# Kernel tuning notes

Hardware: AMD Instinct MI355X
Metric: run time of the kernel (lower is better)

The kernel has to match this reference:

```python
import jax, jax.numpy as jnp
import numpy as np

H = 512      # hidden_size / feature_dim (hard-coded in Net)
H2 = 256     # hidden // 2 in encoder stem
V = 32000    # vocab_size = out_shape[0]
EPS = 1e-5   # BatchNorm eps (torch default)


def _conv(x, w, stride, pad, groups=1):
    return jax.lax.conv_general_dilated(
        x, w, (stride, stride), ((pad, pad), (pad, pad)),
        feature_group_count=groups,
        dimension_numbers=('NCHW', 'OIHW', 'NCHW'))


def _bn(x, g, b):
    # training-mode BatchNorm: biased batch statistics over (N,H,W)
    m = jnp.mean(x, axis=(0, 2, 3), keepdims=True)
    v = jnp.mean((x - m) ** 2, axis=(0, 2, 3), keepdims=True)
    return (x - m) * jax.lax.rsqrt(v + EPS) * g[None, :, None, None] + b[None, :, None, None]


def _encoder(images, conv1_w, bn1_g, bn1_b, dw_w, pw_w, bn2_g, bn2_b,
             se_fc1_w, se_fc2_w, enc_fc_w, enc_fc_b):
    x = jax.nn.relu(_bn(_conv(images, conv1_w, 2, 1), bn1_g, bn1_b))   # [B,256,112,112]
    x = _conv(x, dw_w, 1, 1, groups=H2)                                 # depthwise 3x3
    x = _conv(x, pw_w, 1, 0)                                            # pointwise -> [B,512,112,112]
    x = jax.nn.relu(_bn(x, bn2_g, bn2_b))
    y = jnp.mean(x, axis=(2, 3))                                        # SE squeeze [B,512]
    y = jax.nn.relu(y @ se_fc1_w.T) @ se_fc2_w.T
    x = x * jax.nn.sigmoid(y)[:, :, None, None]                         # SE excite
    f = jnp.mean(x, axis=(2, 3))                                        # AdaptiveAvgPool2d(1)
    return f @ enc_fc_w.T + enc_fc_b                                    # [B,512]


def _decode(feats, inputs, embed, q_w, k_w, v_w,
            gru_w_ih, gru_w_hh, gru_b_ih, gru_b_hh, fc_w, fc_b):
    B = feats.shape[0]
    # Attention over a single feature 'key' (r=1): softmax over one element
    # is exactly 1, so ctx = v(feats), independent of h and of t. q_w/k_w
    # therefore do not influence the output (their gradients are exactly 0).
    ctx = feats @ v_w.T                                                 # [B,512]
    embs = jnp.take(embed, inputs, axis=0)                              # [B,T,512]
    h0 = jnp.zeros((B, H), feats.dtype)

    def step(h, emb_t):
        x = jnp.concatenate([emb_t, ctx], axis=-1)                      # [B,1024]
        gi = x @ gru_w_ih.T + gru_b_ih                                  # [B,1536]
        gh = h @ gru_w_hh.T + gru_b_hh
        ir, iz, inn = jnp.split(gi, 3, axis=-1)
        hr, hz, hn = jnp.split(gh, 3, axis=-1)
        r = jax.nn.sigmoid(ir + hr)
        z = jax.nn.sigmoid(iz + hz)
        n = jnp.tanh(inn + r * hn)
        h_new = (1.0 - z) * n + z * h                                   # torch GRUCell update
        return h_new, h_new @ fc_w.T + fc_b                             # per-step logits [B,V]

    _, logits = jax.lax.scan(step, h0, jnp.swapaxes(embs, 0, 1))        # [T,B,V]
    return jnp.swapaxes(logits, 0, 1)                                   # [B,T,V]


def setup_inputs() -> dict:
    key = jax.random.key(0)
    ks = jax.random.split(key, 16)
    s = 0.02
    B, Tc = 16, 33
    return {
        'images': jax.random.normal(ks[0], (B, 3, 224, 224), jnp.float32),
        'captions': jax.random.randint(ks[1], (B, Tc), 0, V),
        'conv1_w': jax.random.normal(ks[2], (H2, 3, 3, 3), jnp.float32) * s,
        'bn1_g': jnp.ones((H2,), jnp.float32),
        'bn1_b': jnp.zeros((H2,), jnp.float32),
        'dw_w': jax.random.normal(ks[3], (H2, 1, 3, 3), jnp.float32) * s,
        'pw_w': jax.random.normal(ks[4], (H, H2, 1, 1), jnp.float32) * s,
        'bn2_g': jnp.ones((H,), jnp.float32),
        'bn2_b': jnp.zeros((H,), jnp.float32),
        'se_fc1_w': jax.random.normal(ks[5], (H // 4, H), jnp.float32) * s,
        'se_fc2_w': jax.random.normal(ks[6], (H, H // 4), jnp.float32) * s,
        'enc_fc_w': jax.random.normal(ks[7], (H, H), jnp.float32) * s,
        'enc_fc_b': jnp.zeros((H,), jnp.float32),
        'embed': jax.random.normal(ks[8], (V, H), jnp.float32) * s,
        'q_w': jax.random.normal(ks[9], (H, H), jnp.float32) * s,
        'k_w': jax.random.normal(ks[10], (H, H), jnp.float32) * s,
        'v_w': jax.random.normal(ks[11], (H, H), jnp.float32) * s,
        'gru_w_ih': jax.random.normal(ks[12], (3 * H, 2 * H), jnp.float32) * s,
        'gru_w_hh': jax.random.normal(ks[13], (3 * H, H), jnp.float32) * s,
        'gru_b_ih': jnp.zeros((3 * H,), jnp.float32),
        'gru_b_hh': jnp.zeros((3 * H,), jnp.float32),
        'fc_w': jax.random.normal(ks[14], (V, H), jnp.float32) * s,
        'fc_b': jnp.zeros((V,), jnp.float32),
    }


def reference(images, captions, conv1_w, bn1_g, bn1_b, dw_w, pw_w, bn2_g, bn2_b,
              se_fc1_w, se_fc2_w, enc_fc_w, enc_fc_b, embed, q_w, k_w, v_w,
              gru_w_ih, gru_w_hh, gru_b_ih, gru_b_hh, fc_w, fc_b):
    feats = _encoder(images, conv1_w, bn1_g, bn1_b, dw_w, pw_w, bn2_g, bn2_b,
                     se_fc1_w, se_fc2_w, enc_fc_w, enc_fc_b)
    inputs = captions[:, :-1]                                           # teacher forcing
    return _decode(feats, inputs, embed, q_w, k_w, v_w,
                   gru_w_ih, gru_w_hh, gru_b_ih, gru_b_hh, fc_w, fc_b)
```

## Files before the change

kernel.cpp:

```cpp
#include <hip/hip_runtime.h>

typedef unsigned int u32;
typedef unsigned short u16;
typedef unsigned long long u64;
typedef short bf16x8 __attribute__((ext_vector_type(8)));
typedef float f32x4 __attribute__((ext_vector_type(4)));

#define S1 12544
#define NSTAT 200704
#define EPS 1e-5f
#define AP 264

__device__ __forceinline__ u16 f2bf(float f) {
  union { float f; u32 u; } x; x.f = f;
  u32 r = x.u + 0x7fffu + ((x.u >> 16) & 1u);
  return (u16)(r >> 16);
}
__device__ __forceinline__ void bf2x2(u32 u, float& lo, float& hi) {
  union { u32 u; float f; } a, b;
  a.u = u << 16; b.u = u & 0xffff0000u;
  lo = a.f; hi = b.f;
}
__device__ __forceinline__ float sigm(float x) { return 1.f / (1.f + expf(-x)); }

#define CW 225
__global__ __launch_bounds__(256) void k_conv1(const float* __restrict__ img,
    const float* __restrict__ w, u16* __restrict__ out, float* __restrict__ stats) {
  int blk = blockIdx.x;
  int b = blk / 56, strip = blk - b * 56;
  int r0 = strip * 2;
  int c = threadIdx.x;
  __shared__ float simg[3 * 5 * CW];
  const float* ib = img + (size_t)b * 3 * 224 * 224;
  for (int i = c; i < 3 * 5 * CW; i += 256) {
    int ch = i / (5 * CW);
    int rem = i - ch * (5 * CW);
    int lr = rem / CW;
    int col = rem - lr * CW;
    int ih = 2 * r0 - 1 + lr;
    int iw = col - 1;
    float v = 0.f;
    if (ih >= 0 && ih < 224 && iw >= 0 && iw < 224) v = ib[((size_t)ch * 224 + ih) * 224 + iw];
    simg[i] = v;
  }
  float wr[27];
#pragma unroll
  for (int i = 0; i < 27; i++) wr[i] = w[c * 27 + i];
  __syncthreads();
  float s = 0.f, q = 0.f;
  for (int orow = 0; orow < 2; orow++) {
    int oh = r0 + orow;
    for (int ow = 0; ow < 112; ow++) {
      float acc = 0.f;
#pragma unroll
      for (int ch = 0; ch < 3; ch++)
#pragma unroll
        for (int dr = 0; dr < 3; dr++) {
          const float* rp = &simg[(ch * 5 + 2 * orow + dr) * CW + 2 * ow];
          acc = fmaf(wr[(ch * 3 + dr) * 3 + 0], rp[0], acc);
          acc = fmaf(wr[(ch * 3 + dr) * 3 + 1], rp[1], acc);
          acc = fmaf(wr[(ch * 3 + dr) * 3 + 2], rp[2], acc);
        }
      s += acc; q = fmaf(acc, acc, q);
      out[((size_t)(b * 112 + oh) * 112 + ow) * 256 + c] = f2bf(acc);
    }
  }
  atomicAdd(&stats[c], s);
  atomicAdd(&stats[256 + c], q);
}

__global__ void k_bnfin(const float* __restrict__ stats, const float* __restrict__ g,
                        const float* __restrict__ bb, float* __restrict__ par, int C, float invN) {
  int c = blockIdx.x * 256 + threadIdx.x;
  if (c < C) {
    float m = stats[c] * invN;
    float v = stats[C + c] * invN - m * m;
    float sc = g[c] * rsqrtf(v + EPS);
    par[c] = sc;
    par[C + c] = bb[c] - m * sc;
  }
}

__global__ void k_cvt4(const float* __restrict__ w, u16* __restrict__ o, int n4) {
  int i = blockIdx.x * 256 + threadIdx.x;
  if (i < n4) {
    float4 v = ((const float4*)w)[i];
    union { u16 h[4]; uint2 u; } pk;
    pk.h[0] = f2bf(v.x); pk.h[1] = f2bf(v.y); pk.h[2] = f2bf(v.z); pk.h[3] = f2bf(v.w);
    ((uint2*)o)[i] = pk.u;
  }
}

#define LD_COL(ohv, iwv, slot) do {                                          \
    int _oh = (ohv), _iw = (iwv);                                            \
  _Pragma("unroll")                                                          \
    for (int _dr = 0; _dr < 3; _dr++) {                                      \
      int _ih = _oh - 1 + _dr;                                               \
      float _x0 = 0.f, _x1 = 0.f, _x2 = 0.f, _x3 = 0.f;                      \
      if (_ih >= 0 && _ih < 112 && _iw >= 0 && _iw < 112) {                  \
        uint2 _v = *(const uint2*)(ib + ((size_t)(_ih * 112 + _iw)) * 256 + c4); \
        float _t0, _t1, _t2, _t3;                                            \
        bf2x2(_v.x, _t0, _t1); bf2x2(_v.y, _t2, _t3);                        \
        _x0 = fmaxf(fmaf(_t0, sc[0], sh[0]), 0.f);                           \
        _x1 = fmaxf(fmaf(_t1, sc[1], sh[1]), 0.f);                           \
        _x2 = fmaxf(fmaf(_t2, sc[2], sh[2]), 0.f);                           \
        _x3 = fmaxf(fmaf(_t3, sc[3], sh[3]), 0.f);                           \
      }                                                                      \
      act[_dr][slot][0] = _x0; act[_dr][slot][1] = _x1;                      \
      act[_dr][slot][2] = _x2; act[_dr][slot][3] = _x3;                      \
    }                                                                        \
  } while (0)

__global__ __launch_bounds__(256) void k_dws(const u16* __restrict__ cin,
    const float* __restrict__ bn1p, const float* __restrict__ dww, u16* __restrict__ out) {
  int tid = threadIdx.x;
  int wave = tid >> 6, lane = tid & 63;
  int c4 = lane * 4;
  int m0 = blockIdx.x * 64;
  int bimg = blockIdx.x / 196;
  float sc[4], sh[4], w9[4][9];
#pragma unroll
  for (int cc = 0; cc < 4; cc++) {
    sc[cc] = bn1p[c4 + cc];
    sh[cc] = bn1p[256 + c4 + cc];
#pragma unroll
    for (int i = 0; i < 9; i++) w9[cc][i] = dww[(c4 + cc) * 9 + i];
  }
  const u16* ib = cin + (size_t)bimg * S1 * 256;
  float act[3][3][4];
#pragma unroll
  for (int pp = 0; pp < 16; pp++) {
    int p = wave * 16 + pp;
    int s = m0 + p - bimg * S1;
    int oh = s / 112, ow = s - oh * 112;
    if (pp == 0 || ow == 0) {
      LD_COL(oh, ow - 1, (pp + 0) % 3);
      LD_COL(oh, ow,     (pp + 1) % 3);
      LD_COL(oh, ow + 1, (pp + 2) % 3);
    } else {
      LD_COL(oh, ow + 1, (pp + 2) % 3);
    }
    float a0 = 0.f, a1 = 0.f, a2 = 0.f, a3 = 0.f;
#pragma unroll
    for (int dr = 0; dr < 3; dr++)
#pragma unroll
      for (int dc = 0; dc < 3; dc++) {
        const int sl = (pp + dc) % 3;
        const int wi = dr * 3 + dc;
        a0 = fmaf(w9[0][wi], act[dr][sl][0], a0);
        a1 = fmaf(w9[1][wi], act[dr][sl][1], a1);
        a2 = fmaf(w9[2][wi], act[dr][sl][2], a2);
        a3 = fmaf(w9[3][wi], act[dr][sl][3], a3);
      }
    union { u16 h[4]; uint2 v; } pk;
    pk.h[0] = f2bf(a0); pk.h[1] = f2bf(a1);
    pk.h[2] = f2bf(a2); pk.h[3] = f2bf(a3);
    *(uint2*)(out + (size_t)(m0 + p) * 256 + c4) = pk.v;
  }
}

__global__ __launch_bounds__(256, 3) void k_pws(const u16* __restrict__ A,
    const u16* __restrict__ bwb, float* __restrict__ partials,
    const float* __restrict__ bn2p, int pass) {
  __shared__ u16 ash[64 * 256];
  int tid = threadIdx.x;
  int wave = tid >> 6, lane = tid & 63;
  int m0 = blockIdx.x * 64;
  {
    const char* gb = (const char*)(A + (size_t)m0 * 256);
    char* lb = (char*)ash;
#pragma unroll
    for (int i = 0; i < 8; i++) {
      int L = wave * 8192 + i * 1024 + lane * 16;
      int p = L >> 9;
      int gp = (L >> 4) & 31;
      int g = gp ^ (p & 7);
      uint4 v = *(const uint4*)(gb + (size_t)p * 512 + g * 16);
      *(uint4*)(lb + L) = v;
    }
  }
  __syncthreads();

  int quad = lane >> 4;
  int lr = lane & 15;
  int nbase = blockIdx.y * 256 + wave * 64;
  const char* ashb = (const char*)ash;
  f32x4 acc[4][4];
#pragma unroll
  for (int mt = 0; mt < 4; mt++)
#pragma unroll
    for (int nt = 0; nt < 4; nt++) acc[mt][nt] = (f32x4){0.f, 0.f, 0.f, 0.f};

#pragma unroll
  for (int ch = 0; ch < 8; ch++) {
    bf16x8 af[4];
#pragma unroll
    for (int mt = 0; mt < 4; mt++) {
      int row = mt * 16 + lr;
      int g = (ch * 4 + quad) ^ (row & 7);
      af[mt] = *(const bf16x8*)(ashb + row * 512 + g * 16);
    }
    bf16x8 bfr[4];
#pragma unroll
    for (int nt = 0; nt < 4; nt++)
      bfr[nt] = *(const bf16x8*)(bwb + (size_t)(nbase + nt * 16 + lr) * 256 + ch * 32 + quad * 8);
#pragma unroll
    for (int mt = 0; mt < 4; mt++)
#pragma unroll
      for (int nt = 0; nt < 4; nt++)
        acc[mt][nt] = __builtin_amdgcn_mfma_f32_16x16x32_bf16(af[mt], bfr[nt], acc[mt][nt], 0, 0, 0);
  }

  if (pass == 0) {
#pragma unroll
    for (int nt = 0; nt < 4; nt++) {
      float s = 0.f, q = 0.f;
#pragma unroll
      for (int mt = 0; mt < 4; mt++)
#pragma unroll
        for (int r = 0; r < 4; r++) {
          float v = acc[mt][nt][r];
          s += v; q = fmaf(v, v, q);
        }
      s += __shfl_xor(s, 16); s += __shfl_xor(s, 32);
      q += __shfl_xor(q, 16); q += __shfl_xor(q, 32);
      if (lane < 16) {
        int n = nbase + nt * 16 + lane;
        partials[(size_t)blockIdx.x * 1024 + n] = s;
        partials[(size_t)blockIdx.x * 1024 + 512 + n] = q;
      }
    }
  } else {
#pragma unroll
    for (int nt = 0; nt < 4; nt++) {
      int n = nbase + nt * 16 + lr;
      float scn = bn2p[n], shn = bn2p[512 + n];
      float s = 0.f;
#pragma unroll
      for (int mt = 0; mt < 4; mt++)
#pragma unroll
        for (int r = 0; r < 4; r++)
          s += fmaxf(fmaf(acc[mt][nt][r], scn, shn), 0.f);
      s += __shfl_xor(s, 16); s += __shfl_xor(s, 32);
      if (lane < 16)
        partials[(size_t)blockIdx.x * 512 + n] = s;
    }
  }
}

__global__ __launch_bounds__(256, 2) void k_pwpass(
    const u16* __restrict__ conv1out, const float* __restrict__ bn1p,
    const float* __restrict__ dww, const u16* __restrict__ bwb,
    float* __restrict__ partials, const float* __restrict__ bn2p, int pass) {
  __shared__ u16 ash[64 * AP];
  int tid = threadIdx.x;
  int wave = tid >> 6;
  int lane = tid & 63;
  int m0 = blockIdx.x * 64;
  int bimg = blockIdx.x / 196;
  {
    int c4 = lane * 4;
    float sc[4], sh[4], w9[4][9];
#pragma unroll
    for (int cc = 0; cc < 4; cc++) {
      sc[cc] = bn1p[c4 + cc];
      sh[cc] = bn1p[256 + c4 + cc];
#pragma unroll
      for (int i = 0; i < 9; i++) w9[cc][i] = dww[(c4 + cc) * 9 + i];
    }
    const u16* ib = conv1out + (size_t)bimg * S1 * 256;
    float act[3][3][4];
#pragma unroll
    for (int pp = 0; pp < 16; pp++) {
      int p = wave * 16 + pp;
      int s = m0 + p - bimg * S1;
      int oh = s / 112, ow = s - oh * 112;
      if (pp == 0 || ow == 0) {
        LD_COL(oh, ow - 1, (pp + 0) % 3);
        LD_COL(oh, ow,     (pp + 1) % 3);
        LD_COL(oh, ow + 1, (pp + 2) % 3);
      } else {
        LD_COL(oh, ow + 1, (pp + 2) % 3);
      }
      float a0 = 0.f, a1 = 0.f, a2 = 0.f, a3 = 0.f;
#pragma unroll
      for (int dr = 0; dr < 3; dr++)
#pragma unroll
        for (int dc = 0; dc < 3; dc++) {
          const int sl = (pp + dc) % 3;
          const int wi = dr * 3 + dc;
          a0 = fmaf(w9[0][wi], act[dr][sl][0], a0);
          a1 = fmaf(w9[1][wi], act[dr][sl][1], a1);
          a2 = fmaf(w9[2][wi], act[dr][sl][2], a2);
          a3 = fmaf(w9[3][wi], act[dr][sl][3], a3);
        }
      union { u16 h[4]; uint2 v; } pk;
      pk.h[0] = f2bf(a0); pk.h[1] = f2bf(a1);
      pk.h[2] = f2bf(a2); pk.h[3] = f2bf(a3);
      *(uint2*)(&ash[p * AP + c4]) = pk.v;
    }
  }
  __syncthreads();
  int quad = lane >> 4;
  int lr = lane & 15;
  int nbase = wave * 128;
  f32x4 acc[4][8];
#pragma unroll
  for (int mt = 0; mt < 4; mt++)
#pragma unroll
    for (int nt = 0; nt < 8; nt++) acc[mt][nt] = (f32x4){0.f, 0.f, 0.f, 0.f};
  for (int kk = 0; kk < 256; kk += 32) {
    bf16x8 af[4];
#pragma unroll
    for (int mt = 0; mt < 4; mt++)
      af[mt] = *(const bf16x8*)(&ash[(mt * 16 + lr) * AP + kk + quad * 8]);
    bf16x8 bfr[8];
#pragma unroll
    for (int nt = 0; nt < 8; nt++)
      bfr[nt] = *(const bf16x8*)(bwb + (size_t)(nbase + nt * 16 + lr) * 256 + kk + quad * 8);
#pragma unroll
    for (int mt = 0; mt < 4; mt++)
#pragma unroll
      for (int nt = 0; nt < 8; nt++)
        acc[mt][nt] = __builtin_amdgcn_mfma_f32_16x16x32_bf16(af[mt], bfr[nt], acc[mt][nt], 0, 0, 0);
  }
  if (pass == 0) {
#pragma unroll
    for (int nt = 0; nt < 8; nt++) {
      float s = 0.f, q = 0.f;
#pragma unroll
      for (int mt = 0; mt < 4; mt++)
#pragma unroll
        for (int r = 0; r < 4; r++) {
          float v = acc[mt][nt][r];
          s += v; q = fmaf(v, v, q);
        }
      s += __shfl_xor(s, 16); s += __shfl_xor(s, 32);
      q += __shfl_xor(q, 16); q += __shfl_xor(q, 32);
      if (lane < 16) {
        int n = nbase + nt * 16 + lane;
        partials[(size_t)blockIdx.x * 1024 + n] = s;
        partials[(size_t)blockIdx.x * 1024 + 512 + n] = q;
      }
    }
  } else {
#pragma unroll
    for (int nt = 0; nt < 8; nt++) {
      int n = nbase + nt * 16 + lr;
      float scn = bn2p[n], shn = bn2p[512 + n];
      float s = 0.f;
#pragma unroll
      for (int mt = 0; mt < 4; mt++)
#pragma unroll
        for (int r = 0; r < 4; r++)
          s += fmaxf(fmaf(acc[mt][nt][r], scn, shn), 0.f);
      s += __shfl_xor(s, 16); s += __shfl_xor(s, 32);
      if (lane < 16)
        partials[(size_t)blockIdx.x * 512 + n] = s;
    }
  }
}

__global__ __launch_bounds__(256) void k_red1(const float* __restrict__ P, float* __restrict__ P2) {
  int blk = blockIdx.x;
  int t = threadIdx.x;
  float4 s = {0.f, 0.f, 0.f, 0.f};
  for (int r = 0; r < 49; r++) {
    float4 v = *(const float4*)(P + ((size_t)(blk * 49 + r)) * 1024 + t * 4);
    s.x += v.x; s.y += v.y; s.z += v.z; s.w += v.w;
  }
  *(float4*)(P2 + (size_t)blk * 1024 + t * 4) = s;
}

__global__ void k_red_bn2(const float* __restrict__ P2, const float* __restrict__ g,
                          const float* __restrict__ bb, float* __restrict__ par) {
  int c = blockIdx.x * 256 + threadIdx.x;
  float s = 0.f, q = 0.f;
  for (int i = 0; i < 64; i++) {
    s += P2[(size_t)i * 1024 + c];
    q += P2[(size_t)i * 1024 + 512 + c];
  }
  float m = s * (1.f / (float)NSTAT);
  float v = q * (1.f / (float)NSTAT) - m * m;
  float sc = g[c] * rsqrtf(v + EPS);
  par[c] = sc;
  par[512 + c] = bb[c] - m * sc;
}

__global__ void k_red_y(const float* __restrict__ P, float* __restrict__ yb) {
  int idx = blockIdx.x * 256 + threadIdx.x;
  int b = idx >> 9, c = idx & 511;
  float s = 0.f;
  for (int i = 0; i < 196; i++) s += P[(size_t)(b * 196 + i) * 512 + c];
  yb[idx] = s;
}

__global__ __launch_bounds__(256) void k_se(const float* __restrict__ y,
    const float* __restrict__ se1, const float* __restrict__ se2,
    const float* __restrict__ encw, const float* __restrict__ encb,
    const float* __restrict__ vw, float* __restrict__ ctxb) {
  int b = blockIdx.x;
  int t = threadIdx.x;
  __shared__ __align__(16) float ybar[512];
  __shared__ __align__(16) float uu[128];
  __shared__ __align__(16) float ff[512];
  __shared__ __align__(16) float feats[512];
  for (int i = t; i < 512; i += 256) ybar[i] = y[b * 512 + i] * (1.f / 12544.f);
  __syncthreads();
  if (t < 128) {
    const float4* wr = (const float4*)(se1 + t * 512);
    const float4* xv = (const float4*)ybar;
    float a = 0.f;
    for (int k = 0; k < 128; k++) {
      float4 w4 = wr[k], x4 = xv[k];
      a = fmaf(w4.x, x4.x, a); a = fmaf(w4.y, x4.y, a);
      a = fmaf(w4.z, x4.z, a); a = fmaf(w4.w, x4.w, a);
    }
    uu[t] = fmaxf(a, 0.f);
  }
  __syncthreads();
  for (int c = t; c < 512; c += 256) {
    const float4* wr = (const float4*)(se2 + c * 128);
    const float4* xv = (const float4*)uu;
    float a = 0.f;
    for (int k = 0; k < 32; k++) {
      float4 w4 = wr[k], x4 = xv[k];
      a = fmaf(w4.x, x4.x, a); a = fmaf(w4.y, x4.y, a);
      a = fmaf(w4.z, x4.z, a); a = fmaf(w4.w, x4.w, a);
    }
    ff[c] = ybar[c] * sigm(a);
  }
  __syncthreads();
  for (int c = t; c < 512; c += 256) {
    const float4* wr = (const float4*)(encw + (size_t)c * 512);
    const float4* xv = (const float4*)ff;
    float a = encb[c];
    for (int k = 0; k < 128; k++) {
      float4 w4 = wr[k], x4 = xv[k];
      a = fmaf(w4.x, x4.x, a); a = fmaf(w4.y, x4.y, a);
      a = fmaf(w4.z, x4.z, a); a = fmaf(w4.w, x4.w, a);
    }
    feats[c] = a;
  }
  __syncthreads();
  for (int c = t; c < 512; c += 256) {
    const float4* wr = (const float4*)(vw + (size_t)c * 512);
    const float4* xv = (const float4*)feats;
    float a = 0.f;
    for (int k = 0; k < 128; k++) {
      float4 w4 = wr[k], x4 = xv[k];
      a = fmaf(w4.x, x4.x, a); a = fmaf(w4.y, x4.y, a);
      a = fmaf(w4.z, x4.z, a); a = fmaf(w4.w, x4.w, a);
    }
    ctxb[b * 512 + c] = a;
  }
}

__global__ __launch_bounds__(256) void k_gctx(const float* __restrict__ ctxb,
    const float* __restrict__ wih, const float* __restrict__ bih, float* __restrict__ gictx) {
  int lb = threadIdx.x >> 4;
  int lj = threadIdx.x & 15;
  int j = blockIdx.x * 16 + lj;
  const float4* wr = (const float4*)(wih + (size_t)j * 1024 + 512);
  const float4* xv = (const float4*)(ctxb + lb * 512);
  float a = bih[j];
#pragma unroll 4
  for (int k = 0; k < 128; k++) {
    float4 w4 = wr[k], x4 = xv[k];
    a = fmaf(w4.x, x4.x, a); a = fmaf(w4.y, x4.y, a);
    a = fmaf(w4.z, x4.z, a); a = fmaf(w4.w, x4.w, a);
  }
  gictx[lb * 1536 + j] = a;
}

__global__ __launch_bounds__(256) void k_gi3(const int* __restrict__ caps,
    const float* __restrict__ embed, const float* __restrict__ wih,
    const float* __restrict__ gictx, float* __restrict__ gi) {
  int wave = threadIdx.x >> 6, lane = threadIdx.x & 63;
  int j = blockIdx.x * 4 + wave;
  int t0 = blockIdx.y * 8;
  const float4* wr = (const float4*)(wih + (size_t)j * 1024 + lane * 8);
  float4 w0 = wr[0], w1 = wr[1];
  for (int tt = t0; tt < t0 + 8; tt++) {
#pragma unroll
    for (int bb = 0; bb < 16; bb += 8) {
      float4 x0[8], x1[8];
#pragma unroll
      for (int u = 0; u < 8; u++) {
        int tok = caps[(bb + u) * 33 + tt];
        const float4* xv = (const float4*)(embed + (size_t)tok * 512 + lane * 8);
        x0[u] = xv[0]; x1[u] = xv[1];
      }
#pragma unroll
      for (int u = 0; u < 8; u++) {
        float a = w0.x * x0[u].x;
        a = fmaf(w0.y, x0[u].y, a); a = fmaf(w0.z, x0[u].z, a); a = fmaf(w0.w, x0[u].w, a);
        a = fmaf(w1.x, x1[u].x, a); a = fmaf(w1.y, x1[u].y, a);
        a = fmaf(w1.z, x1[u].z, a); a = fmaf(w1.w, x1[u].w, a);
#pragma unroll
        for (int m = 1; m < 64; m <<= 1) a += __shfl_xor(a, m);
        if (lane == 0)
          gi[((size_t)tt * 16 + bb + u) * 1536 + j] = a + gictx[(bb + u) * 1536 + j];
      }
    }
  }
}

__global__ __launch_bounds__(192) void k_gru_step(const float* __restrict__ whh,
    const float* __restrict__ bhh, const float* __restrict__ gi_t,
    const float* __restrict__ h_in, float* __restrict__ h_out) {
  int g = blockIdx.x;
  int tid = threadIdx.x;
  int s = tid / 24;
  int r = tid - s * 24;
  int gate = r >> 3, lj = r & 7;
  int jj = g * 8 + lj;
  int R = gate * 512 + jj;
  float4 w[16];
  {
    const float4* wp = (const float4*)(whh + (size_t)R * 512 + s * 64);
#pragma unroll
    for (int i = 0; i < 16; i++) w[i] = wp[i];
  }
  __shared__ __align__(16) float hs[16][512];
  __shared__ float pr[8][24][16];

  {
    const float4* hp = (const float4*)h_in;
    float4* hd = (float4*)&hs[0][0];
    for (int i = tid; i < 2048; i += 192) hd[i] = hp[i];
  }
  __syncthreads();
#pragma unroll
  for (int b = 0; b < 16; b++) {
    const float4* hv = (const float4*)&hs[b][s * 64];
    float a = 0.f;
#pragma unroll
    for (int k = 0; k < 16; k++) {
      float4 w4 = w[k], h4 = hv[k];
      a = fmaf(w4.x, h4.x, a); a = fmaf(w4.y, h4.y, a);
      a = fmaf(w4.z, h4.z, a); a = fmaf(w4.w, h4.w, a);
    }
    pr[s][r][b] = a;
  }
  __syncthreads();
  if (tid < 128) {
    int b = tid >> 3, jl = tid & 7;
    int j = g * 8 + jl;
    float gh[3];
#pragma unroll
    for (int gg = 0; gg < 3; gg++) {
      int rr = gg * 8 + jl;
      float sum = bhh[gg * 512 + j];
#pragma unroll
      for (int ss = 0; ss < 8; ss++) sum += pr[ss][rr][b];
      gh[gg] = sum;
    }
    const float* gib = gi_t + (size_t)b * 1536;
    float rg = sigm(gib[j] + gh[0]);
    float z  = sigm(gib[j + 512] + gh[1]);
    float n  = tanhf(gib[j + 1024] + rg * gh[2]);
    float hp = hs[b][j];
    h_out[b * 512 + j] = (1.f - z) * n + z * hp;
  }
}

__global__ __launch_bounds__(256) void k_fc(const float* __restrict__ A,
    const u16* __restrict__ Bwb, const float* __restrict__ bias, float* __restrict__ out) {
  __shared__ u16 ash[128 * 136];
  int tid = threadIdx.x;
  int wave = tid >> 6;
  int lane = tid & 63;
  int quad = lane >> 4;
  int lr = lane & 15;
  int N0 = blockIdx.x * 256;
  int M0 = blockIdx.y * 128;
  f32x4 acc[8][4];
#pragma unroll
  for (int mf = 0; mf < 8; mf++)
#pragma unroll
    for (int nf = 0; nf < 4; nf++) acc[mf][nf] = (f32x4){0.f, 0.f, 0.f, 0.f};
  int arow = tid >> 1;
  int acol = (tid & 1) * 64;
  for (int kc = 0; kc < 512; kc += 128) {
#pragma unroll
    for (int j = 0; j < 16; j++) {
      float4 v = *(const float4*)(A + (size_t)(M0 + arow) * 512 + kc + acol + j * 4);
      union { u16 h[4]; uint2 u; } pk;
      pk.h[0] = f2bf(v.x); pk.h[1] = f2bf(v.y); pk.h[2] = f2bf(v.z); pk.h[3] = f2bf(v.w);
      *(uint2*)(&ash[arow * 136 + acol + j * 4]) = pk.u;
    }
    __syncthreads();
#pragma unroll
    for (int ks = 0; ks < 128; ks += 32) {
      bf16x8 af[8];
#pragma unroll
      for (int mf = 0; mf < 8; mf++)
        af[mf] = *(const bf16x8*)(&ash[(mf * 16 + lr) * 136 + ks + quad * 8]);
      bf16x8 bf[4];
#pragma unroll
      for (int nf = 0; nf < 4; nf++) {
        int n = N0 + wave * 64 + nf * 16 + lr;
        bf[nf] = *(const bf16x8*)(Bwb + (size_t)n * 512 + kc + ks + quad * 8);
      }
#pragma unroll
      for (int mf = 0; mf < 8; mf++)
#pragma unroll
        for (int nf = 0; nf < 4; nf++)
          acc[mf][nf] = __builtin_amdgcn_mfma_f32_16x16x32_bf16(af[mf], bf[nf], acc[mf][nf], 0, 0, 0);
    }
    __syncthreads();
  }
#pragma unroll
  for (int nf = 0; nf < 4; nf++) {
    int j = N0 + wave * 64 + nf * 16 + lr;
    float bv = bias[j];
#pragma unroll
    for (int mf = 0; mf < 8; mf++)
#pragma unroll
      for (int r = 0; r < 4; r++) {
        int m = M0 + mf * 16 + quad * 4 + r;
        int orow = (m & 15) * 32 + (m >> 4);
        out[(size_t)orow * 32000 + j] = acc[mf][nf][r] + bv;
      }
  }
}

extern "C" void kernel_launch(void* const* d_in, const int* in_sizes, int n_in,
                              void* d_out, int out_size, void* d_ws, size_t ws_size,
                              hipStream_t stream) {
  const float* images  = (const float*)d_in[0];
  const int*   caps    = (const int*)d_in[1];
  const float* conv1_w = (const float*)d_in[2];
  const float* bn1_g   = (const float*)d_in[3];
  const float* bn1_b   = (const float*)d_in[4];
  const float* dw_w    = (const float*)d_in[5];
  const float* pw_w    = (const float*)d_in[6];
  const float* bn2_g   = (const float*)d_in[7];
  const float* bn2_b   = (const float*)d_in[8];
  const float* se1     = (const float*)d_in[9];
  const float* se2     = (const float*)d_in[10];
  const float* encw    = (const float*)d_in[11];
  const float* encb    = (const float*)d_in[12];
  const float* embed   = (const float*)d_in[13];
  const float* vw      = (const float*)d_in[16];
  const float* wih     = (const float*)d_in[17];
  const float* whh     = (const float*)d_in[18];
  const float* bih     = (const float*)d_in[19];
  const float* bhh     = (const float*)d_in[20];
  const float* fcw     = (const float*)d_in[21];
  const float* fcb     = (const float*)d_in[22];
  float* out = (float*)d_out;

  const bool big = ws_size >= (size_t)230 * 1000 * 1000;

  char* ws = (char*)d_ws;
  size_t off = 0;
  auto alloc = [&](size_t bytes) {
    void* p = ws + off;
    off = (off + bytes + 255) & ~(size_t)255;
    return p;
  };
  u16* conv1out = (u16*)alloc((size_t)51380224 * 2);
  u16* fcwb     = (u16*)conv1out;
  u16* dwout    = big ? (u16*)alloc((size_t)51380224 * 2) : (u16*)nullptr;
  u16* bwb      = (u16*)alloc((size_t)131072 * 2);
  float* partials = (float*)alloc((size_t)3136 * 1024 * 4);
  float* p2     = (float*)alloc((size_t)64 * 1024 * 4);
  float* stats1 = (float*)alloc(512 * 4);
  float* h_all  = (float*)alloc((size_t)33 * 8192 * 4);
  float* bn1p   = (float*)alloc(512 * 4);
  float* bn2p   = (float*)alloc(1024 * 4);
  float* yb     = (float*)alloc(8192 * 4);
  float* ctxb   = (float*)alloc(8192 * 4);
  float* gictx  = (float*)alloc((size_t)16 * 1536 * 4);
  float* gi     = (float*)alloc((size_t)32 * 16 * 1536 * 4);
  (void)in_sizes; (void)n_in; (void)out_size;

  hipMemsetAsync(stats1, 0, 512 * 4, stream);
  hipMemsetAsync(h_all, 0, 8192 * 4, stream);

  k_conv1<<<896, 256, 0, stream>>>(images, conv1_w, conv1out, stats1);
  k_bnfin<<<1, 256, 0, stream>>>(stats1, bn1_g, bn1_b, bn1p, 256, 1.f / (float)NSTAT);
  k_cvt4<<<128, 256, 0, stream>>>(pw_w, bwb, 32768);

  if (big) {
    k_dws<<<3136, 256, 0, stream>>>(conv1out, bn1p, dw_w, dwout);
    k_cvt4<<<16000, 256, 0, stream>>>(fcw, fcwb, 4096000);
    dim3 gpw(3136, 2);
    k_pws<<<gpw, 256, 0, stream>>>(dwout, bwb, partials, bn2p, 0);
    k_red1<<<64, 256, 0, stream>>>(partials, p2);
    k_red_bn2<<<2, 256, 0, stream>>>(p2, bn2_g, bn2_b, bn2p);
    k_pws<<<gpw, 256, 0, stream>>>(dwout, bwb, partials, bn2p, 1);
  } else {
    k_pwpass<<<3136, 256, 0, stream>>>(conv1out, bn1p, dw_w, bwb, partials, bn2p, 0);
    k_red1<<<64, 256, 0, stream>>>(partials, p2);
    k_red_bn2<<<2, 256, 0, stream>>>(p2, bn2_g, bn2_b, bn2p);
    k_pwpass<<<3136, 256, 0, stream>>>(conv1out, bn1p, dw_w, bwb, partials, bn2p, 1);
    k_cvt4<<<16000, 256, 0, stream>>>(fcw, fcwb, 4096000);
  }
  k_red_y<<<32, 256, 0, stream>>>(partials, yb);
  k_se<<<16, 256, 0, stream>>>(yb, se1, se2, encw, encb, vw, ctxb);
  k_gctx<<<96, 256, 0, stream>>>(ctxb, wih, bih, gictx);
  dim3 ggi3(384, 4);
  k_gi3<<<ggi3, 256, 0, stream>>>(caps, embed, wih, gictx, gi);
  for (int t = 0; t < 32; t++)
    k_gru_step<<<64, 192, 0, stream>>>(whh, bhh, gi + (size_t)t * 16 * 1536,
                                       h_all + (size_t)t * 8192, h_all + (size_t)(t + 1) * 8192);
  dim3 gfc(125, 4);
  k_fc<<<gfc, 256, 0, stream>>>(h_all + 8192, fcwb, fcb, out);
}
```

Measured before the change: 1.273 ms.

## Transpose GRU input weights and rewrite embedding projection as LDS-staged GEMM

Adds a transpose kernel that lays out the embedding half of W_ih as [k][j]. The embedding projection is rewritten so each thread owns one output column and accumulates all 16 batch rows. The gathered embeddings are staged in shared memory, and weight reads are coalesced across lanes. This removes the per-output 64-lane shuffle reductions of the old kernel. The cost is an extra transpose pass, a 3MB buffer, and a grid of only 192 blocks, each running a 512-step serial loop.

```diff
diff --git a/kernel.cpp b/kernel.cpp
--- a/kernel.cpp
+++ b/kernel.cpp
@@ -108,7 +108,7 @@
       }                                                                      \
       act[_dr][slot][0] = _x0; act[_dr][slot][1] = _x1;                      \
       act[_dr][slot][2] = _x2; act[_dr][slot][3] = _x3;                      \
-    }                                                                        \
+    }                                                                      \
   } while (0)
 
 __global__ __launch_bounds__(256) void k_dws(const u16* __restrict__ cin,
@@ -473,37 +473,58 @@
   gictx[lb * 1536 + j] = a;
 }
 
-__global__ __launch_bounds__(256) void k_gi3(const int* __restrict__ caps,
-    const float* __restrict__ embed, const float* __restrict__ wih,
+__global__ __launch_bounds__(256) void k_trans(const float* __restrict__ wih,
+    float* __restrict__ wihT) {
+  __shared__ float tile[32][33];
+  int tx = threadIdx.x & 31, ty = threadIdx.x >> 5;
+  int j0 = blockIdx.x * 32, k0 = blockIdx.y * 32;
+#pragma unroll
+  for (int i = 0; i < 4; i++)
+    tile[ty + i * 8][tx] = wih[(size_t)(j0 + ty + i * 8) * 1024 + k0 + tx];
+  __syncthreads();
+#pragma unroll
+  for (int i = 0; i < 4; i++)
+    wihT[(size_t)(k0 + ty + i * 8) * 1536 + j0 + tx] = tile[tx][ty + i * 8];
+}
+
+__global__ __launch_bounds__(256) void k_gi4(const int* __restrict__ caps,
+    const float* __restrict__ embed, const float* __restrict__ wihT,
     const float* __restrict__ gictx, float* __restrict__ gi) {
-  int wave = threadIdx.x >> 6, lane = threadIdx.x & 63;
-  int j = blockIdx.x * 4 + wave;
-  int t0 = blockIdx.y * 8;
-  const float4* wr = (const float4*)(wih + (size_t)j * 1024 + lane * 8);
-  float4 w0 = wr[0], w1 = wr[1];
-  for (int tt = t0; tt < t0 + 8; tt++) {
-#pragma unroll
-    for (int bb = 0; bb < 16; bb += 8) {
-      float4 x0[8], x1[8];
-#pragma unroll
-      for (int u = 0; u < 8; u++) {
-        int tok = caps[(bb + u) * 33 + tt];
-        const float4* xv = (const float4*)(embed + (size_t)tok * 512 + lane * 8);
-        x0[u] = xv[0]; x1[u] = xv[1];
-      }
-#pragma unroll
-      for (int u = 0; u < 8; u++) {
-        float a = w0.x * x0[u].x;
-        a = fmaf(w0.y, x0[u].y, a); a = fmaf(w0.z, x0[u].z, a); a = fmaf(w0.w, x0[u].w, a);
-        a = fmaf(w1.x, x1[u].x, a); a = fmaf(w1.y, x1[u].y, a);
-        a = fmaf(w1.z, x1[u].z, a); a = fmaf(w1.w, x1[u].w, a);
-#pragma unroll
-        for (int m = 1; m < 64; m <<= 1) a += __shfl_xor(a, m);
-        if (lane == 0)
-          gi[((size_t)tt * 16 + bb + u) * 1536 + j] = a + gictx[(bb + u) * 1536 + j];
-      }
-    }
-  }
+  __shared__ __align__(16) float semb[512][16];
+  int tid = threadIdx.x;
+  int t = blockIdx.y;
+  for (int i = tid; i < 8192; i += 256) {
+    int k = i >> 4, b = i & 15;
+    int tok = caps[b * 33 + t];
+    semb[k][b] = embed[(size_t)tok * 512 + k];
+  }
+  __syncthreads();
+  int wave = tid >> 6, lane = tid & 63;
+  int j = (blockIdx.x * 4 + wave) * 64 + lane;
+  float acc[16];
+#pragma unroll
+  for (int b = 0; b < 16; b++) acc[b] = 0.f;
+  for (int k = 0; k < 512; k += 2) {
+    float wv0 = wihT[(size_t)k * 1536 + j];
+    float wv1 = wihT[(size_t)(k + 1) * 1536 + j];
+    const f32x4* e0 = (const f32x4*)&semb[k][0];
+    const f32x4* e1 = (const f32x4*)&semb[k + 1][0];
+#pragma unroll
+    for (int q = 0; q < 4; q++) {
+      f32x4 a0 = e0[q], a1 = e1[q];
+      acc[q * 4 + 0] = fmaf(wv0, a0[0], acc[q * 4 + 0]);
+      acc[q * 4 + 1] = fmaf(wv0, a0[1], acc[q * 4 + 1]);
+      acc[q * 4 + 2] = fmaf(wv0, a0[2], acc[q * 4 + 2]);
+      acc[q * 4 + 3] = fmaf(wv0, a0[3], acc[q * 4 + 3]);
+      acc[q * 4 + 0] = fmaf(wv1, a1[0], acc[q * 4 + 0]);
+      acc[q * 4 + 1] = fmaf(wv1, a1[1], acc[q * 4 + 1]);
+      acc[q * 4 + 2] = fmaf(wv1, a1[2], acc[q * 4 + 2]);
+      acc[q * 4 + 3] = fmaf(wv1, a1[3], acc[q * 4 + 3]);
+    }
+  }
+#pragma unroll
+  for (int b = 0; b < 16; b++)
+    gi[((size_t)t * 16 + b) * 1536 + j] = acc[b] + gictx[b * 1536 + j];
 }
 
 __global__ __launch_bounds__(192) void k_gru_step(const float* __restrict__ whh,
@@ -674,6 +695,7 @@
   float* yb     = (float*)alloc(8192 * 4);
   float* ctxb   = (float*)alloc(8192 * 4);
   float* gictx  = (float*)alloc((size_t)16 * 1536 * 4);
+  float* wihT   = (float*)alloc((size_t)512 * 1536 * 4);
   float* gi     = (float*)alloc((size_t)32 * 16 * 1536 * 4);
   (void)in_sizes; (void)n_in; (void)out_size;
 
@@ -683,6 +705,10 @@
   k_conv1<<<896, 256, 0, stream>>>(images, conv1_w, conv1out, stats1);
   k_bnfin<<<1, 256, 0, stream>>>(stats1, bn1_g, bn1_b, bn1p, 256, 1.f / (float)NSTAT);
   k_cvt4<<<128, 256, 0, stream>>>(pw_w, bwb, 32768);
+  {
+    dim3 gtr(48, 16);
+    k_trans<<<gtr, 256, 0, stream>>>(wih, wihT);
+  }
 
   if (big) {
     k_dws<<<3136, 256, 0, stream>>>(conv1out, bn1p, dw_w, dwout);
@@ -702,8 +728,8 @@
   k_red_y<<<32, 256, 0, stream>>>(partials, yb);
   k_se<<<16, 256, 0, stream>>>(yb, se1, se2, encw, encb, vw, ctxb);
   k_gctx<<<96, 256, 0, stream>>>(ctxb, wih, bih, gictx);
-  dim3 ggi3(384, 4);
-  k_gi3<<<ggi3, 256, 0, stream>>>(caps, embed, wih, gictx, gi);
+  dim3 ggi4(6, 32);
+  k_gi4<<<ggi4, 256, 0, stream>>>(caps, embed, wihT, gictx, gi);
   for (int t = 0; t < 32; t++)
     k_gru_step<<<64, 192, 0, stream>>>(whh, bhh, gi + (size_t)t * 16 * 1536,
                                        h_all + (size_t)t * 8192, h_all + (size_t)(t + 1) * 8192);
```

New measurement: 1.236 ms. 1.03x faster.
